# Performance work log

Measured on AMD Instinct MI355X. Metric: run time of the kernel, lower is better.

The kernel has to match this reference:

```python
import jax, jax.numpy as jnp
import numpy as np
import math

B, S, H = 2, 2048, 3072
NH, NKV, HD = 32, 32, 96
BASE = 10000.0
NEG = -1e9


def rotate_half(x):
    x1 = x[..., : x.shape[-1] // 2]
    x2 = x[..., x.shape[-1] // 2 :]
    return jnp.concatenate((-x2, x1), axis=-1)


def setup_inputs() -> dict:
    key = jax.random.key(0)
    k1, k2, k3 = jax.random.split(key, 3)
    hidden_states = jax.random.normal(k1, (B, S, H), dtype=jnp.float32)
    position_ids = jnp.broadcast_to(jnp.arange(S, dtype=jnp.int32), (B, S))
    # additive causal mask: 0 where key <= query, -1e9 above the diagonal
    i = jnp.arange(S)
    causal = jnp.where(i[None, :] <= i[:, None], 0.0, NEG).astype(jnp.float32)
    attention_mask = jnp.broadcast_to(causal[None, None], (B, 1, S, S))
    w_qkv = jax.random.normal(k2, (NH * HD + 2 * NKV * HD, H), dtype=jnp.float32) * 0.02
    w_o = jax.random.normal(k3, (H, NH * HD), dtype=jnp.float32) * 0.02
    return {
        "hidden_states": hidden_states,
        "position_ids": position_ids,
        "attention_mask": attention_mask,
        "w_qkv": w_qkv,
        "w_o": w_o,
    }


def reference(hidden_states, position_ids, attention_mask, w_qkv, w_o):
    bsz, q_len, _ = hidden_states.shape
    # fused QKV projection (no bias), then split per Phi3 layout
    qkv = jnp.einsum("bsh,oh->bso", hidden_states, w_qkv)
    q = qkv[..., : NH * HD]
    k = qkv[..., NH * HD : NH * HD + NKV * HD]
    v = qkv[..., NH * HD + NKV * HD :]
    q = q.reshape(bsz, q_len, NH, HD).transpose(0, 2, 1, 3)   # [B,NH,S,HD]
    k = k.reshape(bsz, q_len, NKV, HD).transpose(0, 2, 1, 3)  # [B,NKV,S,HD]
    v = v.reshape(bsz, q_len, NKV, HD).transpose(0, 2, 1, 3)

    # rotary embeddings (Phi3RotaryEmbedding, no scaling)
    inv_freq = 1.0 / (BASE ** (jnp.arange(0, HD, 2, dtype=jnp.float32) / HD))  # [HD/2]
    freqs = position_ids.astype(jnp.float32)[:, :, None] * inv_freq[None, None, :]  # [B,S,HD/2]
    emb = jnp.concatenate((freqs, freqs), axis=-1)  # [B,S,HD]
    cos = jnp.cos(emb)[:, None].astype(hidden_states.dtype)  # [B,1,S,HD]
    sin = jnp.sin(emb)[:, None].astype(hidden_states.dtype)
    q = q * cos + rotate_half(q) * sin
    k = k * cos + rotate_half(k) * sin
    # num_key_value_groups = NH // NKV = 1 -> repeat_kv is a no-op

    attn = jnp.einsum("bhqd,bhkd->bhqk", q, k) / math.sqrt(HD)
    attn = attn + attention_mask  # broadcast over heads
    attn = jax.nn.softmax(attn.astype(jnp.float32), axis=-1).astype(v.dtype)
    # attention_dropout = 0.0 / eval mode -> dropout is identity
    out = jnp.einsum("bhqk,bhkd->bhqd", attn, v)
    out = out.transpose(0, 2, 1, 3).reshape(bsz, q_len, NH * HD)
    return jnp.einsum("bso,ho->bsh", out, w_o)
```

## Files before the change

### kernel.cpp

```cpp
#include <hip/hip_runtime.h>
#include <hip/hip_bf16.h>
#include <type_traits>

typedef unsigned short ushort_t;
typedef __attribute__((ext_vector_type(8))) short bf16x8;
typedef __attribute__((ext_vector_type(4))) float f32x4;

#define S_LEN 2048
#define NHEAD 32
#define HDIM 96

__device__ __forceinline__ float bf2f(ushort_t b) {
    union { unsigned u; float f; } v; v.u = ((unsigned)b) << 16; return v.f;
}
__device__ __forceinline__ ushort_t f2bf(float f) {
    union { float f; unsigned u; } v; v.f = f;
    unsigned r = v.u + 0x7fffu + ((v.u >> 16) & 1u);
    return (ushort_t)(r >> 16);
}
__device__ __forceinline__ void cp16(ushort_t* l, const ushort_t* g) {
    __builtin_amdgcn_global_load_lds((const __attribute__((address_space(1))) void*)g,
                                     (__attribute__((address_space(3))) void*)l, 16, 0, 0);
}

__global__ void cvt_f32_bf16(const float* __restrict__ src, ushort_t* __restrict__ dst, int n8)
{
    const int i = blockIdx.x * 256 + threadIdx.x;
    if (i >= n8) return;
    const float4 a = ((const float4*)src)[2 * i];
    const float4 b = ((const float4*)src)[2 * i + 1];
    union { ushort_t us[8]; int4 v; } r;
    r.us[0] = f2bf(a.x); r.us[1] = f2bf(a.y); r.us[2] = f2bf(a.z); r.us[3] = f2bf(a.w);
    r.us[4] = f2bf(b.x); r.us[5] = f2bf(b.y); r.us[6] = f2bf(b.z); r.us[7] = f2bf(b.w);
    ((int4*)dst)[i] = r.v;
}

template <typename OT>
__global__ __launch_bounds__(256, 3) void gemm_bt(
    const ushort_t* __restrict__ A, const ushort_t* __restrict__ Bm,
    OT* __restrict__ C, int M, int N, int K)
{
    __shared__ ushort_t As[128 * 32];
    __shared__ ushort_t Bs[128 * 32];
    const int tid = threadIdx.x;
    const int m0 = blockIdx.y * 128, n0 = blockIdx.x * 128;
    const int w = tid >> 6, lane = tid & 63;
    const int wm = w >> 1, wn = w & 1;
    const int r16 = lane & 15, quad = lane >> 4;

    f32x4 acc[4][4];
#pragma unroll
    for (int i = 0; i < 4; i++)
#pragma unroll
        for (int j = 0; j < 4; j++) acc[i][j] = f32x4{0.f, 0.f, 0.f, 0.f};

    const ushort_t* ga = A + (size_t)(m0 + (tid >> 2)) * K + (tid & 3) * 8;
    const ushort_t* gb = Bm + (size_t)(n0 + (tid >> 2)) * K + (tid & 3) * 8;
    ushort_t* la = As + tid * 8;
    ushort_t* lb = Bs + tid * 8;
    const size_t rowskip = (size_t)64 * K;

    for (int k0 = 0; k0 < K; k0 += 32) {
        __syncthreads();
        cp16(la,        ga);
        cp16(la + 2048, ga + rowskip);
        cp16(lb,        gb);
        cp16(lb + 2048, gb + rowskip);
        ga += 32; gb += 32;
        __syncthreads();
        bf16x8 av[4], bv[4];
#pragma unroll
        for (int i = 0; i < 4; i++)
            av[i] = *(const bf16x8*)&As[(64 * wm + 16 * i + r16) * 32 + quad * 8];
#pragma unroll
        for (int j = 0; j < 4; j++)
            bv[j] = *(const bf16x8*)&Bs[(64 * wn + 16 * j + r16) * 32 + quad * 8];
#pragma unroll
        for (int i = 0; i < 4; i++)
#pragma unroll
            for (int j = 0; j < 4; j++)
                acc[i][j] = __builtin_amdgcn_mfma_f32_16x16x32_bf16(av[i], bv[j], acc[i][j], 0, 0, 0);
    }
#pragma unroll
    for (int i = 0; i < 4; i++) {
        const int row0 = m0 + 64 * wm + 16 * i + quad * 4;
#pragma unroll
        for (int j = 0; j < 4; j++) {
            const int col = n0 + 64 * wn + 16 * j + r16;
#pragma unroll
            for (int r = 0; r < 4; r++) {
                if constexpr (std::is_same<OT, float>::value)
                    C[(size_t)(row0 + r) * N + col] = acc[i][j][r];
                else
                    C[(size_t)(row0 + r) * N + col] = f2bf(acc[i][j][r]);
            }
        }
    }
}

__global__ void rope_scatter(const ushort_t* __restrict__ qkv, const int* __restrict__ pos,
                             ushort_t* __restrict__ Q, ushort_t* __restrict__ Kd)
{
    const int d = threadIdx.x;
    const int t = blockIdx.x * 2 + threadIdx.y;
    const int h = blockIdx.y;
    const int which = d >= 48;
    const int dd = which ? d - 48 : d;
    const int p = pos[t];
    const float inv = exp2f((float)dd * (-13.287712379549449f / 48.0f));
    const float th = (float)p * inv;
    const float cs = cosf(th), sn = sinf(th);
    const ushort_t* src = qkv + (size_t)t * 9216 + (which ? 3072 : 0) + h * 96;
    const float x1 = bf2f(src[dd]), x2 = bf2f(src[dd + 48]);
    ushort_t* dst = (which ? Kd : Q) +
        ((size_t)((t >> 11) * NHEAD + h) * S_LEN + (t & 2047)) * HDIM;
    dst[dd]      = f2bf(x1 * cs - x2 * sn);
    dst[dd + 48] = f2bf(x2 * cs + x1 * sn);
}

__global__ void v_transpose(const ushort_t* __restrict__ qkv, ushort_t* __restrict__ VT)
{
    const int t = blockIdx.x * 64 + threadIdx.x;
    const int h = blockIdx.y;
    const int d = blockIdx.z * 8 + threadIdx.y;
    const int b = t >> 11, s = t & 2047;
    VT[((size_t)(b * NHEAD + h) * HDIM + d) * S_LEN + s] =
        qkv[(size_t)t * 9216 + 6144 + h * 96 + d];
}

__global__ __launch_bounds__(256, 2) void flash_attn(
    const ushort_t* __restrict__ Q, const ushort_t* __restrict__ Kg,
    const ushort_t* __restrict__ VT, ushort_t* __restrict__ attn)
{
    __shared__ ushort_t Qs[128 * 104];
    __shared__ ushort_t Ps[128 * 72];

    const int tid = threadIdx.x, w = tid >> 6, lane = tid & 63;
    const int r16 = lane & 15, quad = lane >> 4;
    const int qi = 15 - (blockIdx.x >> 6);
    const int bh = blockIdx.x & 63;
    const int q0 = qi * 128;
    const ushort_t* Qg  = Q  + ((size_t)bh * S_LEN + q0) * HDIM;
    const ushort_t* Kgb = Kg + (size_t)bh * S_LEN * HDIM;
    const ushort_t* Vgb = VT + (size_t)bh * HDIM * S_LEN;

#pragma unroll
    for (int c = 0; c < 6; c++) {
        const int cc = tid + 256 * c;
        const int row = cc / 12, col = (cc % 12) * 8;
        *(int4*)&Qs[row * 104 + col] = *(const int4*)(Qg + row * 96 + col);
    }
    __syncthreads();

    float m_st[2][4], l_st[2][4];
#pragma unroll
    for (int i = 0; i < 2; i++)
#pragma unroll
        for (int r = 0; r < 4; r++) { m_st[i][r] = -1.0e30f; l_st[i][r] = 0.f; }

    f32x4 o[2][6];
#pragma unroll
    for (int i = 0; i < 2; i++)
#pragma unroll
        for (int jo = 0; jo < 6; jo++) o[i][jo] = f32x4{0.f, 0.f, 0.f, 0.f};

    const float sc = 0.10206207261596577f;
    const float L2E = 1.4426950408889634f;
    const int nkt = 2 * qi + 2;
    const int rowb = 32 * w;

    for (int kt = 0; kt < nkt; ++kt) {
        const int k0 = kt * 64;

        f32x4 sacc[2][4];
#pragma unroll
        for (int i = 0; i < 2; i++)
#pragma unroll
            for (int j = 0; j < 4; j++) sacc[i][j] = f32x4{0.f, 0.f, 0.f, 0.f};
#pragma unroll
        for (int kk = 0; kk < 3; kk++) {
            bf16x8 qa[2], kb[4];
#pragma unroll
            for (int i = 0; i < 2; i++)
                qa[i] = *(const bf16x8*)&Qs[(rowb + 16 * i + r16) * 104 + kk * 32 + quad * 8];
#pragma unroll
            for (int j = 0; j < 4; j++)
                kb[j] = *(const bf16x8*)(Kgb + (size_t)(k0 + 16 * j + r16) * 96
                                         + kk * 32 + quad * 8);
#pragma unroll
            for (int i = 0; i < 2; i++)
#pragma unroll
                for (int j = 0; j < 4; j++)
                    sacc[i][j] = __builtin_amdgcn_mfma_f32_16x16x32_bf16(qa[i], kb[j], sacc[i][j], 0, 0, 0);
        }

        const bool need_mask = (kt >= 2 * qi);
#pragma unroll
        for (int i = 0; i < 2; i++)
#pragma unroll
            for (int j = 0; j < 4; j++)
#pragma unroll
                for (int r = 0; r < 4; r++) {
                    float v = sacc[i][j][r] * sc;
                    if (need_mask) {
                        const int grow = q0 + rowb + 16 * i + quad * 4 + r;
                        const int gcol = k0 + 16 * j + r16;
                        if (gcol > grow) v = -1.0e9f;
                    }
                    sacc[i][j][r] = v;
                }

        float mt[2][4];
#pragma unroll
        for (int i = 0; i < 2; i++)
#pragma unroll
            for (int r = 0; r < 4; r++) {
                float mp = fmaxf(fmaxf(sacc[i][0][r], sacc[i][1][r]),
                                 fmaxf(sacc[i][2][r], sacc[i][3][r]));
                mp = fmaxf(mp, __shfl_xor(mp, 1, 16));
                mp = fmaxf(mp, __shfl_xor(mp, 2, 16));
                mp = fmaxf(mp, __shfl_xor(mp, 4, 16));
                mp = fmaxf(mp, __shfl_xor(mp, 8, 16));
                mt[i][r] = mp;
            }

        float alpha[2][4];
#pragma unroll
        for (int i = 0; i < 2; i++)
#pragma unroll
            for (int r = 0; r < 4; r++) {
                const float mn = fmaxf(m_st[i][r], mt[i][r]);
                alpha[i][r] = exp2f((m_st[i][r] - mn) * L2E);
                m_st[i][r] = mn;
            }

        float psum[2][4];
#pragma unroll
        for (int i = 0; i < 2; i++)
#pragma unroll
            for (int r = 0; r < 4; r++) psum[i][r] = 0.f;
#pragma unroll
        for (int i = 0; i < 2; i++)
#pragma unroll
            for (int j = 0; j < 4; j++)
#pragma unroll
                for (int r = 0; r < 4; r++) {
                    const float p = exp2f((sacc[i][j][r] - m_st[i][r]) * L2E);
                    psum[i][r] += p;
                    Ps[(rowb + 16 * i + quad * 4 + r) * 72 + 16 * j + r16] = f2bf(p);
                }
#pragma unroll
        for (int i = 0; i < 2; i++)
#pragma unroll
            for (int r = 0; r < 4; r++) {
                float s2 = psum[i][r];
                s2 += __shfl_xor(s2, 1, 16);
                s2 += __shfl_xor(s2, 2, 16);
                s2 += __shfl_xor(s2, 4, 16);
                s2 += __shfl_xor(s2, 8, 16);
                l_st[i][r] = l_st[i][r] * alpha[i][r] + s2;
            }

#pragma unroll
        for (int i = 0; i < 2; i++)
#pragma unroll
            for (int jo = 0; jo < 6; jo++)
#pragma unroll
                for (int r = 0; r < 4; r++) o[i][jo][r] *= alpha[i][r];
#pragma unroll
        for (int kk = 0; kk < 2; kk++) {
            bf16x8 pa[2], vb[6];
#pragma unroll
            for (int i = 0; i < 2; i++)
                pa[i] = *(const bf16x8*)&Ps[(rowb + 16 * i + r16) * 72 + kk * 32 + quad * 8];
#pragma unroll
            for (int jo = 0; jo < 6; jo++)
                vb[jo] = *(const bf16x8*)(Vgb + (size_t)(16 * jo + r16) * S_LEN
                                          + k0 + kk * 32 + quad * 8);
#pragma unroll
            for (int i = 0; i < 2; i++)
#pragma unroll
                for (int jo = 0; jo < 6; jo++)
                    o[i][jo] = __builtin_amdgcn_mfma_f32_16x16x32_bf16(pa[i], vb[jo], o[i][jo], 0, 0, 0);
        }
    }

    const int b = bh >> 5, h = bh & 31;
#pragma unroll
    for (int i = 0; i < 2; i++)
#pragma unroll
        for (int r = 0; r < 4; r++) {
            const int lr = rowb + 16 * i + quad * 4 + r;
            const float inv = 1.0f / l_st[i][r];
            const size_t base = (size_t)(b * S_LEN + q0 + lr) * 3072 + h * 96;
#pragma unroll
            for (int jo = 0; jo < 6; jo++)
                attn[base + 16 * jo + r16] = f2bf(o[i][jo][r] * inv);
        }
}

extern "C" void kernel_launch(void* const* d_in, const int* in_sizes, int n_in,
                              void* d_out, int out_size, void* d_ws, size_t ws_size,
                              hipStream_t stream)
{
    const float* hidden = (const float*)d_in[0];
    const int*   pos    = (const int*)d_in[1];
    const float* w_qkv  = (const float*)d_in[3];
    const float* w_o    = (const float*)d_in[4];
    float* out          = (float*)d_out;

    char* ws = (char*)d_ws;
    ushort_t* hbf    = (ushort_t*)(ws);
    ushort_t* wqkvbf = (ushort_t*)(ws + 25165824);
    ushort_t* Qb     = (ushort_t*)(ws);
    ushort_t* Kb     = (ushort_t*)(ws + 25165824);
    ushort_t* VTb    = (ushort_t*)(ws + 50331648);
    ushort_t* qkv    = (ushort_t*)(ws + 81788928);
    ushort_t* attn   = qkv;
    ushort_t* wobf   = (ushort_t*)(ws + 157286400);

    cvt_f32_bf16<<<dim3(12582912 / 8 / 256), 256, 0, stream>>>(hidden, hbf, 12582912 / 8);
    cvt_f32_bf16<<<dim3(28311552 / 8 / 256), 256, 0, stream>>>(w_qkv, wqkvbf, 28311552 / 8);
    cvt_f32_bf16<<<dim3(9437184 / 8 / 256), 256, 0, stream>>>(w_o, wobf, 9437184 / 8);

    gemm_bt<ushort_t><<<dim3(72, 32), 256, 0, stream>>>(hbf, wqkvbf, qkv, 4096, 9216, 3072);
    rope_scatter<<<dim3(2048, 32), dim3(96, 2), 0, stream>>>(qkv, pos, Qb, Kb);
    v_transpose<<<dim3(64, 32, 12), dim3(64, 8), 0, stream>>>(qkv, VTb);
    flash_attn<<<dim3(1024), 256, 0, stream>>>(Qb, Kb, VTb, attn);
    gemm_bt<float><<<dim3(24, 32), 256, 0, stream>>>(attn, wobf, out, 4096, 3072, 3072);
}
```

Baseline: 830.6 us.

## Replace GEMM with 256x256-tile double-buffered pipelined MFMA kernel

Replaces the 128x128 single-buffered GEMM with a 256x256 tile, 512-thread kernel. It double-buffers K=64 slabs in LDS, interleaves async global->LDS loads with MFMA phases using explicit waitcnt, barriers and setprio, XOR-swizzles the LDS layout to avoid bank conflicts, and remaps workgroups for L2 locality. The goal is to hide global load latency and raise data reuse per tile for both projection GEMMs. The trade-offs are heavier register use (32 accumulators per thread) and fewer workgroups, only 192 blocks for the output GEMM.

```diff
diff --git a/kernel.cpp b/kernel.cpp
--- a/kernel.cpp
+++ b/kernel.cpp
@@ -36,63 +36,158 @@
 }
 
 template <typename OT>
-__global__ __launch_bounds__(256, 3) void gemm_bt(
+__global__ __launch_bounds__(512, 2) void gemm256(
     const ushort_t* __restrict__ A, const ushort_t* __restrict__ Bm,
     OT* __restrict__ C, int M, int N, int K)
 {
-    __shared__ ushort_t As[128 * 32];
-    __shared__ ushort_t Bs[128 * 32];
+    __shared__ ushort_t As[2][2][8192];
+    __shared__ ushort_t Bs[2][2][8192];
     const int tid = threadIdx.x;
-    const int m0 = blockIdx.y * 128, n0 = blockIdx.x * 128;
-    const int w = tid >> 6, lane = tid & 63;
-    const int wm = w >> 1, wn = w & 1;
+    const int lane = tid & 63, w = tid >> 6;
+    const int wm = w >> 2, wn = w & 3;
     const int r16 = lane & 15, quad = lane >> 4;
 
-    f32x4 acc[4][4];
-#pragma unroll
-    for (int i = 0; i < 4; i++)
-#pragma unroll
-        for (int j = 0; j < 4; j++) acc[i][j] = f32x4{0.f, 0.f, 0.f, 0.f};
-
-    const ushort_t* ga = A + (size_t)(m0 + (tid >> 2)) * K + (tid & 3) * 8;
-    const ushort_t* gb = Bm + (size_t)(n0 + (tid >> 2)) * K + (tid & 3) * 8;
-    ushort_t* la = As + tid * 8;
-    ushort_t* lb = Bs + tid * 8;
-    const size_t rowskip = (size_t)64 * K;
-
-    for (int k0 = 0; k0 < K; k0 += 32) {
-        __syncthreads();
-        cp16(la,        ga);
-        cp16(la + 2048, ga + rowskip);
-        cp16(lb,        gb);
-        cp16(lb + 2048, gb + rowskip);
-        ga += 32; gb += 32;
-        __syncthreads();
-        bf16x8 av[4], bv[4];
-#pragma unroll
-        for (int i = 0; i < 4; i++)
-            av[i] = *(const bf16x8*)&As[(64 * wm + 16 * i + r16) * 32 + quad * 8];
-#pragma unroll
-        for (int j = 0; j < 4; j++)
-            bv[j] = *(const bf16x8*)&Bs[(64 * wn + 16 * j + r16) * 32 + quad * 8];
-#pragma unroll
-        for (int i = 0; i < 4; i++)
-#pragma unroll
-            for (int j = 0; j < 4; j++)
-                acc[i][j] = __builtin_amdgcn_mfma_f32_16x16x32_bf16(av[i], bv[j], acc[i][j], 0, 0, 0);
+    const int gx = gridDim.x;
+    const int nwg = gx * gridDim.y;
+    const int bid = blockIdx.y * gx + blockIdx.x;
+    const int swz = (bid & 7) * (nwg >> 3) + (bid >> 3);
+    const int n0 = (swz % gx) * 256;
+    const int m0 = (swz / gx) * 256;
+
+    const int srow = tid >> 2;
+    const int scol = ((tid & 3) ^ ((tid >> 3) & 3)) * 8;
+    const ushort_t* gA = A + (size_t)(m0 + srow) * K + scol;
+    const ushort_t* gB = Bm + (size_t)(n0 + srow) * K + scol;
+    const size_t rsk = (size_t)128 * K;
+
+    const int laneoff = r16 * 32 + (quad ^ ((r16 >> 1) & 3)) * 8;
+
+    f32x4 acc[8][4];
+#pragma unroll
+    for (int m = 0; m < 8; m++)
+#pragma unroll
+        for (int n = 0; n < 4; n++) acc[m][n] = f32x4{0.f, 0.f, 0.f, 0.f};
+
+    const int NT = K >> 6;
+
+    cp16(&As[0][0][tid * 8],        gA);
+    cp16(&As[0][0][tid * 8 + 4096], gA + rsk);
+    cp16(&Bs[0][0][tid * 8],        gB);
+    cp16(&Bs[0][0][tid * 8 + 4096], gB + rsk);
+    cp16(&As[0][1][tid * 8],        gA + 32);
+    cp16(&As[0][1][tid * 8 + 4096], gA + rsk + 32);
+    cp16(&Bs[0][1][tid * 8],        gB + 32);
+    cp16(&Bs[0][1][tid * 8 + 4096], gB + rsk + 32);
+    cp16(&As[1][0][tid * 8],        gA + 64);
+    cp16(&As[1][0][tid * 8 + 4096], gA + rsk + 64);
+    cp16(&Bs[1][0][tid * 8],        gB + 64);
+    cp16(&Bs[1][0][tid * 8 + 4096], gB + rsk + 64);
+    asm volatile("s_waitcnt vmcnt(8)" ::: "memory");
+    __builtin_amdgcn_s_barrier();
+
+#pragma unroll 2
+    for (int t = 0; t < NT; ++t) {
+        const int b = t & 1, bn = b ^ 1;
+        const int kb = t << 6;
+        bf16x8 afr[4], bfr[4];
+
+#pragma unroll
+        for (int n = 0; n < 4; n++)
+            bfr[n] = *(const bf16x8*)&Bs[b][0][(wn * 64 + n * 16) * 32 + laneoff];
+#pragma unroll
+        for (int mm = 0; mm < 4; mm++)
+            afr[mm] = *(const bf16x8*)&As[b][0][(wm * 128 + mm * 16) * 32 + laneoff];
+        if (t + 1 < NT) {
+            cp16(&As[bn][1][tid * 8],        gA + kb + 96);
+            cp16(&As[bn][1][tid * 8 + 4096], gA + rsk + kb + 96);
+        }
+        __builtin_amdgcn_s_barrier();
+        asm volatile("s_waitcnt lgkmcnt(0)" ::: "memory");
+        __builtin_amdgcn_s_setprio(1);
+#pragma unroll
+        for (int mm = 0; mm < 4; mm++)
+#pragma unroll
+            for (int n = 0; n < 4; n++)
+                acc[mm][n] = __builtin_amdgcn_mfma_f32_16x16x32_bf16(afr[mm], bfr[n], acc[mm][n], 0, 0, 0);
+        __builtin_amdgcn_s_setprio(0);
+        __builtin_amdgcn_s_barrier();
+
+#pragma unroll
+        for (int mm = 0; mm < 4; mm++)
+            afr[mm] = *(const bf16x8*)&As[b][0][(wm * 128 + 64 + mm * 16) * 32 + laneoff];
+        if (t + 1 < NT) {
+            cp16(&Bs[bn][1][tid * 8],        gB + kb + 96);
+            cp16(&Bs[bn][1][tid * 8 + 4096], gB + rsk + kb + 96);
+            asm volatile("s_waitcnt vmcnt(8)" ::: "memory");
+        } else {
+            asm volatile("s_waitcnt vmcnt(0)" ::: "memory");
+        }
+        __builtin_amdgcn_s_barrier();
+        asm volatile("s_waitcnt lgkmcnt(0)" ::: "memory");
+        __builtin_amdgcn_s_setprio(1);
+#pragma unroll
+        for (int mm = 0; mm < 4; mm++)
+#pragma unroll
+            for (int n = 0; n < 4; n++)
+                acc[4 + mm][n] = __builtin_amdgcn_mfma_f32_16x16x32_bf16(afr[mm], bfr[n], acc[4 + mm][n], 0, 0, 0);
+        __builtin_amdgcn_s_setprio(0);
+        __builtin_amdgcn_s_barrier();
+
+#pragma unroll
+        for (int n = 0; n < 4; n++)
+            bfr[n] = *(const bf16x8*)&Bs[b][1][(wn * 64 + n * 16) * 32 + laneoff];
+#pragma unroll
+        for (int mm = 0; mm < 4; mm++)
+            afr[mm] = *(const bf16x8*)&As[b][1][(wm * 128 + mm * 16) * 32 + laneoff];
+        if (t + 2 < NT) {
+            cp16(&As[b][0][tid * 8],        gA + kb + 128);
+            cp16(&As[b][0][tid * 8 + 4096], gA + rsk + kb + 128);
+        }
+        __builtin_amdgcn_s_barrier();
+        asm volatile("s_waitcnt lgkmcnt(0)" ::: "memory");
+        __builtin_amdgcn_s_setprio(1);
+#pragma unroll
+        for (int mm = 0; mm < 4; mm++)
+#pragma unroll
+            for (int n = 0; n < 4; n++)
+                acc[mm][n] = __builtin_amdgcn_mfma_f32_16x16x32_bf16(afr[mm], bfr[n], acc[mm][n], 0, 0, 0);
+        __builtin_amdgcn_s_setprio(0);
+        __builtin_amdgcn_s_barrier();
+
+#pragma unroll
+        for (int mm = 0; mm < 4; mm++)
+            afr[mm] = *(const bf16x8*)&As[b][1][(wm * 128 + 64 + mm * 16) * 32 + laneoff];
+        if (t + 2 < NT) {
+            cp16(&Bs[b][0][tid * 8],        gB + kb + 128);
+            cp16(&Bs[b][0][tid * 8 + 4096], gB + rsk + kb + 128);
+            asm volatile("s_waitcnt vmcnt(8)" ::: "memory");
+        } else if (t + 1 < NT) {
+            asm volatile("s_waitcnt vmcnt(4)" ::: "memory");
+        }
+        __builtin_amdgcn_s_barrier();
+        asm volatile("s_waitcnt lgkmcnt(0)" ::: "memory");
+        __builtin_amdgcn_s_setprio(1);
+#pragma unroll
+        for (int mm = 0; mm < 4; mm++)
+#pragma unroll
+            for (int n = 0; n < 4; n++)
+                acc[4 + mm][n] = __builtin_amdgcn_mfma_f32_16x16x32_bf16(afr[mm], bfr[n], acc[4 + mm][n], 0, 0, 0);
+        __builtin_amdgcn_s_setprio(0);
+        __builtin_amdgcn_s_barrier();
     }
-#pragma unroll
-    for (int i = 0; i < 4; i++) {
-        const int row0 = m0 + 64 * wm + 16 * i + quad * 4;
-#pragma unroll
-        for (int j = 0; j < 4; j++) {
-            const int col = n0 + 64 * wn + 16 * j + r16;
+
+#pragma unroll
+    for (int m = 0; m < 8; m++) {
+        const int row0 = m0 + wm * 128 + m * 16 + quad * 4;
+#pragma unroll
+        for (int n = 0; n < 4; n++) {
+            const int col = n0 + wn * 64 + n * 16 + r16;
 #pragma unroll
             for (int r = 0; r < 4; r++) {
                 if constexpr (std::is_same<OT, float>::value)
-                    C[(size_t)(row0 + r) * N + col] = acc[i][j][r];
+                    C[(size_t)(row0 + r) * N + col] = acc[m][n][r];
                 else
-                    C[(size_t)(row0 + r) * N + col] = f2bf(acc[i][j][r]);
+                    C[(size_t)(row0 + r) * N + col] = f2bf(acc[m][n][r]);
             }
         }
     }
@@ -323,9 +418,9 @@
     cvt_f32_bf16<<<dim3(28311552 / 8 / 256), 256, 0, stream>>>(w_qkv, wqkvbf, 28311552 / 8);
     cvt_f32_bf16<<<dim3(9437184 / 8 / 256), 256, 0, stream>>>(w_o, wobf, 9437184 / 8);
 
-    gemm_bt<ushort_t><<<dim3(72, 32), 256, 0, stream>>>(hbf, wqkvbf, qkv, 4096, 9216, 3072);
+    gemm256<ushort_t><<<dim3(36, 16), 512, 0, stream>>>(hbf, wqkvbf, qkv, 4096, 9216, 3072);
     rope_scatter<<<dim3(2048, 32), dim3(96, 2), 0, stream>>>(qkv, pos, Qb, Kb);
     v_transpose<<<dim3(64, 32, 12), dim3(64, 8), 0, stream>>>(qkv, VTb);
     flash_attn<<<dim3(1024), 256, 0, stream>>>(Qb, Kb, VTb, attn);
-    gemm_bt<float><<<dim3(24, 32), 256, 0, stream>>>(attn, wobf, out, 4096, 3072, 3072);
-}
+    gemm256<float><<<dim3(12, 16), 512, 0, stream>>>(attn, wobf, out, 4096, 3072, 3072);
+}
```

After: 860.3 us. 3.6% more time.

## Replace GEMM with 256x192 double-buffered tiles, swizzled LDS, and 8 waves

Applied to the files above, without the earlier changes.

Both projection GEMMs now use a new kernel with 512 threads, 256x192 output tiles and a K step of 64. LDS is double-buffered and XOR-swizzled, and loads are split into half-tile stages with explicit vmcnt waits and setprio around the MFMA bursts. The goal is more data reuse per LDS load, fewer bank conflicts, and global loads that overlap compute instead of the old load-sync-compute loop over 128x128 tiles. The cost is higher register and LDS pressure and fragile hand-counted waitcnt logic. The output GEMM gets only 256 blocks, which may underfill the GPU.

```diff
diff --git a/kernel.cpp b/kernel.cpp
--- a/kernel.cpp
+++ b/kernel.cpp
@@ -36,63 +36,119 @@
 }
 
 template <typename OT>
-__global__ __launch_bounds__(256, 3) void gemm_bt(
+__global__ __launch_bounds__(512, 2) void gemm256(
     const ushort_t* __restrict__ A, const ushort_t* __restrict__ Bm,
     OT* __restrict__ C, int M, int N, int K)
 {
-    __shared__ ushort_t As[128 * 32];
-    __shared__ ushort_t Bs[128 * 32];
+    __shared__ ushort_t As[2][16384];
+    __shared__ ushort_t Bs[2][12288];
     const int tid = threadIdx.x;
-    const int m0 = blockIdx.y * 128, n0 = blockIdx.x * 128;
-    const int w = tid >> 6, lane = tid & 63;
-    const int wm = w >> 1, wn = w & 1;
+    const int lane = tid & 63, w = tid >> 6;
+    const int wm = w >> 2, wn = w & 3;
     const int r16 = lane & 15, quad = lane >> 4;
 
-    f32x4 acc[4][4];
-#pragma unroll
-    for (int i = 0; i < 4; i++)
-#pragma unroll
-        for (int j = 0; j < 4; j++) acc[i][j] = f32x4{0.f, 0.f, 0.f, 0.f};
-
-    const ushort_t* ga = A + (size_t)(m0 + (tid >> 2)) * K + (tid & 3) * 8;
-    const ushort_t* gb = Bm + (size_t)(n0 + (tid >> 2)) * K + (tid & 3) * 8;
-    ushort_t* la = As + tid * 8;
-    ushort_t* lb = Bs + tid * 8;
-    const size_t rowskip = (size_t)64 * K;
-
-    for (int k0 = 0; k0 < K; k0 += 32) {
-        __syncthreads();
-        cp16(la,        ga);
-        cp16(la + 2048, ga + rowskip);
-        cp16(lb,        gb);
-        cp16(lb + 2048, gb + rowskip);
-        ga += 32; gb += 32;
-        __syncthreads();
-        bf16x8 av[4], bv[4];
-#pragma unroll
-        for (int i = 0; i < 4; i++)
-            av[i] = *(const bf16x8*)&As[(64 * wm + 16 * i + r16) * 32 + quad * 8];
-#pragma unroll
-        for (int j = 0; j < 4; j++)
-            bv[j] = *(const bf16x8*)&Bs[(64 * wn + 16 * j + r16) * 32 + quad * 8];
-#pragma unroll
-        for (int i = 0; i < 4; i++)
-#pragma unroll
-            for (int j = 0; j < 4; j++)
-                acc[i][j] = __builtin_amdgcn_mfma_f32_16x16x32_bf16(av[i], bv[j], acc[i][j], 0, 0, 0);
+    const int m0 = blockIdx.y * 256;
+    const int n0 = blockIdx.x * 192;
+
+    const int sl8 = ((tid & 3) ^ ((tid >> 3) & 3)) * 8;
+    const int srow = tid >> 2;
+    const ushort_t* gA  = A  + (size_t)(m0 + srow) * K + sl8;
+    const size_t rsk = (size_t)128 * K;
+    const ushort_t* gB0 = Bm + (size_t)(n0 + srow) * K + sl8;
+    const ushort_t* gB1 = Bm + (size_t)(n0 + ((tid < 256) ? (128 + srow) : ((tid - 256) >> 2))) * K
+                          + ((tid < 256) ? 0 : 32) + sl8;
+    const ushort_t* gB2 = Bm + (size_t)(n0 + 64 + srow) * K + 32 + sl8;
+
+    const int laneoff = r16 * 32 + (quad ^ ((r16 >> 1) & 3)) * 8;
+
+    f32x4 acc[8][3];
+#pragma unroll
+    for (int m = 0; m < 8; m++)
+#pragma unroll
+        for (int j = 0; j < 3; j++) acc[m][j] = f32x4{0.f, 0.f, 0.f, 0.f};
+
+    const int NT = K >> 6;
+
+#define STAGE_B(bn, kb)  { cp16(&Bs[bn][tid * 8],         gB0 + (kb)); \
+                           cp16(&Bs[bn][tid * 8 + 4096],  gB1 + (kb)); \
+                           cp16(&Bs[bn][tid * 8 + 8192],  gB2 + (kb)); }
+#define STAGE_A0(bn, kb) { cp16(&As[bn][tid * 8],         gA + (kb)); \
+                           cp16(&As[bn][tid * 8 + 4096],  gA + rsk + (kb)); }
+#define STAGE_A1(bn, kb) { cp16(&As[bn][tid * 8 + 8192],  gA + (kb) + 32); \
+                           cp16(&As[bn][tid * 8 + 12288], gA + rsk + (kb) + 32); }
+
+    STAGE_B(0, 0);
+    STAGE_A0(0, 0);
+    STAGE_A1(0, 0);
+    asm volatile("s_waitcnt vmcnt(2)" ::: "memory");
+    __builtin_amdgcn_s_barrier();
+
+    for (int t = 0; t < NT; ++t) {
+        const int b = t & 1, bn = b ^ 1;
+        const int kb = (t + 1) << 6;
+        bf16x8 av[8], bv[3];
+
+#pragma unroll
+        for (int j = 0; j < 3; j++)
+            bv[j] = *(const bf16x8*)&Bs[b][(wn * 48 + j * 16) * 32 + laneoff];
+#pragma unroll
+        for (int m = 0; m < 8; m++)
+            av[m] = *(const bf16x8*)&As[b][(wm * 128 + m * 16) * 32 + laneoff];
+        if (t + 1 < NT) {
+            STAGE_B(bn, kb);
+            STAGE_A0(bn, kb);
+        }
+        __builtin_amdgcn_s_barrier();
+        __builtin_amdgcn_s_setprio(1);
+#pragma unroll
+        for (int m = 0; m < 8; m++)
+#pragma unroll
+            for (int j = 0; j < 3; j++)
+                acc[m][j] = __builtin_amdgcn_mfma_f32_16x16x32_bf16(av[m], bv[j], acc[m][j], 0, 0, 0);
+        __builtin_amdgcn_s_setprio(0);
+        if (t + 1 < NT) {
+            asm volatile("s_waitcnt vmcnt(5)" ::: "memory");
+        } else {
+            asm volatile("s_waitcnt vmcnt(0)" ::: "memory");
+        }
+        __builtin_amdgcn_s_barrier();
+
+#pragma unroll
+        for (int j = 0; j < 3; j++)
+            bv[j] = *(const bf16x8*)&Bs[b][6144 + (wn * 48 + j * 16) * 32 + laneoff];
+#pragma unroll
+        for (int m = 0; m < 8; m++)
+            av[m] = *(const bf16x8*)&As[b][8192 + (wm * 128 + m * 16) * 32 + laneoff];
+        if (t + 1 < NT) {
+            STAGE_A1(bn, kb);
+        }
+        __builtin_amdgcn_s_barrier();
+        __builtin_amdgcn_s_setprio(1);
+#pragma unroll
+        for (int m = 0; m < 8; m++)
+#pragma unroll
+            for (int j = 0; j < 3; j++)
+                acc[m][j] = __builtin_amdgcn_mfma_f32_16x16x32_bf16(av[m], bv[j], acc[m][j], 0, 0, 0);
+        __builtin_amdgcn_s_setprio(0);
+        asm volatile("s_waitcnt vmcnt(2)" ::: "memory");
+        __builtin_amdgcn_s_barrier();
     }
-#pragma unroll
-    for (int i = 0; i < 4; i++) {
-        const int row0 = m0 + 64 * wm + 16 * i + quad * 4;
-#pragma unroll
-        for (int j = 0; j < 4; j++) {
-            const int col = n0 + 64 * wn + 16 * j + r16;
+#undef STAGE_B
+#undef STAGE_A0
+#undef STAGE_A1
+
+#pragma unroll
+    for (int m = 0; m < 8; m++) {
+        const int row0 = m0 + wm * 128 + m * 16 + quad * 4;
+#pragma unroll
+        for (int j = 0; j < 3; j++) {
+            const int col = n0 + wn * 48 + j * 16 + r16;
 #pragma unroll
             for (int r = 0; r < 4; r++) {
                 if constexpr (std::is_same<OT, float>::value)
-                    C[(size_t)(row0 + r) * N + col] = acc[i][j][r];
+                    C[(size_t)(row0 + r) * N + col] = acc[m][j][r];
                 else
-                    C[(size_t)(row0 + r) * N + col] = f2bf(acc[i][j][r]);
+                    C[(size_t)(row0 + r) * N + col] = f2bf(acc[m][j][r]);
             }
         }
     }
@@ -323,9 +379,9 @@
     cvt_f32_bf16<<<dim3(28311552 / 8 / 256), 256, 0, stream>>>(w_qkv, wqkvbf, 28311552 / 8);
     cvt_f32_bf16<<<dim3(9437184 / 8 / 256), 256, 0, stream>>>(w_o, wobf, 9437184 / 8);
 
-    gemm_bt<ushort_t><<<dim3(72, 32), 256, 0, stream>>>(hbf, wqkvbf, qkv, 4096, 9216, 3072);
+    gemm256<ushort_t><<<dim3(48, 16), 512, 0, stream>>>(hbf, wqkvbf, qkv, 4096, 9216, 3072);
     rope_scatter<<<dim3(2048, 32), dim3(96, 2), 0, stream>>>(qkv, pos, Qb, Kb);
     v_transpose<<<dim3(64, 32, 12), dim3(64, 8), 0, stream>>>(qkv, VTb);
     flash_attn<<<dim3(1024), 256, 0, stream>>>(Qb, Kb, VTb, attn);
-    gemm_bt<float><<<dim3(24, 32), 256, 0, stream>>>(attn, wobf, out, 4096, 3072, 3072);
-}
+    gemm256<float><<<dim3(16, 16), 512, 0, stream>>>(attn, wobf, out, 4096, 3072, 3072);
+}
```

Result: no change. 846.1 us (+1.9%).
